# Optimization experiments

Measured on AMD Instinct MI355X. Metric: run time of the kernel, lower is better.

Reference implementation:

```python
import jax, jax.numpy as jnp
import numpy as np

EPS = 1e-6
HEADS = 8

def _ln_cf(x, w, b):
    # ConvNeXt-style channels_first LayerNorm over C axis of (B,C,H,W)
    mu = jnp.mean(x, axis=1, keepdims=True)
    var = jnp.mean((x - mu) ** 2, axis=1, keepdims=True)
    xn = (x - mu) / jnp.sqrt(var + EPS)
    return xn * w[None, :, None, None] + b[None, :, None, None]

def _xattn(q_map, kv_map, Wq, Wk, Wv, Wo, bo):
    B, C, H, W = q_map.shape
    HW = H * W
    dh = C // HEADS
    xq = q_map.reshape(B, C, HW).transpose(0, 2, 1)   # (B,HW,C)
    xkv = kv_map.reshape(B, C, HW).transpose(0, 2, 1)
    q = (xq @ Wq.T).reshape(B, HW, HEADS, dh).transpose(0, 2, 1, 3)
    k = (xkv @ Wk.T).reshape(B, HW, HEADS, dh).transpose(0, 2, 1, 3)
    v = (xkv @ Wv.T).reshape(B, HW, HEADS, dh).transpose(0, 2, 1, 3)
    scale = dh ** -0.5
    logits = jnp.einsum('bhqd,bhkd->bhqk', q, k) * scale
    attn = jax.nn.softmax(logits, axis=-1)
    o = jnp.einsum('bhqk,bhkd->bhqd', attn, v)        # (B,h,HW,dh)
    o = o.transpose(0, 2, 1, 3).reshape(B, HW, C)
    o = o @ Wo.T + bo
    return o.transpose(0, 2, 1).reshape(B, C, H, W)

def _ffn(x, W1, b1, W2, b2):
    # 1x1 convs == channel-wise linear; exact GELU (torch default)
    h = jnp.einsum('bchw,oc->bohw', x, W1) + b1[None, :, None, None]
    h = jax.nn.gelu(h, approximate=False)
    return jnp.einsum('bchw,oc->bohw', h, W2) + b2[None, :, None, None]

def setup_inputs() -> dict:
    key = jax.random.key(0)
    ks = jax.random.split(key, 24)
    B, C, H, W = 8, 512, 32, 32
    hid = 4 * C
    d = {
        'spatial_feat': jax.random.normal(ks[0], (B, C, H, W), jnp.float32),
        'freq_feat': jax.random.normal(ks[1], (B, C, H, W), jnp.float32),
        # spatial enhancer (standard cross-attn)
        's_Wq': jax.random.normal(ks[2], (C, C), jnp.float32) * 0.02,
        's_Wk': jax.random.normal(ks[3], (C, C), jnp.float32) * 0.02,
        's_Wv': jax.random.normal(ks[4], (C, C), jnp.float32) * 0.02,
        's_Wo': jax.random.normal(ks[5], (C, C), jnp.float32) * 0.02,
        's_bo': jnp.zeros((C,), jnp.float32),
        # frequency enhancer
        'f_Wq': jax.random.normal(ks[6], (C, C), jnp.float32) * 0.02,
        'f_Wk': jax.random.normal(ks[7], (C, C), jnp.float32) * 0.02,
        'f_Wv': jax.random.normal(ks[8], (C, C), jnp.float32) * 0.02,
        'f_Wo': jax.random.normal(ks[9], (C, C), jnp.float32) * 0.02,
        'f_bo': jnp.zeros((C,), jnp.float32),
        # norms
        'sn1_w': jnp.ones((C,), jnp.float32), 'sn1_b': jnp.zeros((C,), jnp.float32),
        'sn2_w': jnp.ones((C,), jnp.float32), 'sn2_b': jnp.zeros((C,), jnp.float32),
        'fn1_w': jnp.ones((C,), jnp.float32), 'fn1_b': jnp.zeros((C,), jnp.float32),
        'fn2_w': jnp.ones((C,), jnp.float32), 'fn2_b': jnp.zeros((C,), jnp.float32),
        # ConvFFNs (1x1 convs)
        'sffn_W1': jax.random.normal(ks[10], (hid, C), jnp.float32) * 0.02,
        'sffn_b1': jnp.zeros((hid,), jnp.float32),
        'sffn_W2': jax.random.normal(ks[11], (C, hid), jnp.float32) * 0.02,
        'sffn_b2': jnp.zeros((C,), jnp.float32),
        'fffn_W1': jax.random.normal(ks[12], (hid, C), jnp.float32) * 0.02,
        'fffn_b1': jnp.zeros((hid,), jnp.float32),
        'fffn_W2': jax.random.normal(ks[13], (C, hid), jnp.float32) * 0.02,
        'fffn_b2': jnp.zeros((C,), jnp.float32),
    }
    return d

def reference(spatial_feat, freq_feat,
              s_Wq, s_Wk, s_Wv, s_Wo, s_bo,
              f_Wq, f_Wk, f_Wv, f_Wo, f_bo,
              sn1_w, sn1_b, sn2_w, sn2_b,
              fn1_w, fn1_b, fn2_w, fn2_b,
              sffn_W1, sffn_b1, sffn_W2, sffn_b2,
              fffn_W1, fffn_b1, fffn_W2, fffn_b2):
    enh_s = _xattn(spatial_feat, freq_feat, s_Wq, s_Wk, s_Wv, s_Wo, s_bo)
    enh_f = _xattn(freq_feat, spatial_feat, f_Wq, f_Wk, f_Wv, f_Wo, f_bo)
    s = _ln_cf(spatial_feat + enh_s, sn1_w, sn1_b)
    s = _ln_cf(s + _ffn(s, sffn_W1, sffn_b1, sffn_W2, sffn_b2), sn2_w, sn2_b)
    f = _ln_cf(freq_feat + enh_f, fn1_w, fn1_b)
    f = _ln_cf(f + _ffn(f, fffn_W1, fffn_b1, fffn_W2, fffn_b2), fn2_w, fn2_b)
    return (s, f)
```

## Files before the change

kernel.cpp:

```cpp
#include <hip/hip_runtime.h>
#include <hip/hip_bf16.h>


#define CCH 512
#define HWD 1024

typedef unsigned short u16;
typedef unsigned int u32;
typedef __attribute__((ext_vector_type(8))) __bf16 bf16x8;
typedef __attribute__((ext_vector_type(4))) float f32x4;
typedef __attribute__((ext_vector_type(4))) unsigned short u16x4;
typedef __attribute__((ext_vector_type(8))) unsigned short u16x8;

__device__ __forceinline__ float bf2f(u16 u) { return __uint_as_float(((u32)u) << 16); }
__device__ __forceinline__ u16 f2bf(float f) {
    u32 u = __float_as_uint(f);
    return (u16)((u + 0x7fffu + ((u >> 16) & 1u)) >> 16);
}
__device__ __forceinline__ float ldp(const void* p, int i, bool isbf) {
    return isbf ? bf2f(((const u16*)p)[i]) : ((const float*)p)[i];
}

#define GLL16(g, l) __builtin_amdgcn_global_load_lds( \
    (const __attribute__((address_space(1))) u32*)(g), \
    (__attribute__((address_space(3))) u32*)(l), 16, 0, 0)

struct MMJob { const u16* A; const u16* W; const void* bias; void* Y; };
struct AJob  { const u16* QK; const u16* VT; u16* AO; };
struct LNJob { const u16* A; const float* Br; const void* w; const void* b; void* Y; };

__global__ void k_detect(const u16* __restrict__ in, int* __restrict__ flag) {
    if (threadIdx.x == 0 && blockIdx.x == 0) {
        int sane = 0;
        for (int i = 0; i < 1024; i += 2) {
            int e = (in[i] >> 7) & 0xFF;
            if (e >= 0x6D && e <= 0x8D) sane++;
        }
        *flag = (sane >= 256) ? 1 : 0;
    }
}

struct CvtJobs {
    const void* src[12];
    u16* dst[12];
    int chunk0[13];
};
__global__ __launch_bounds__(256) void k_cvt_all(CvtJobs J, const int* __restrict__ flag) {
    bool isbf = (*flag != 0);
    int b = blockIdx.x;
    int j = 0;
    #pragma unroll
    for (int i = 0; i < 12; i++) if (b >= J.chunk0[i + 1]) j = i + 1;
    int idx = (b - J.chunk0[j]) * 1024 + threadIdx.x * 4;
    u16* d = J.dst[j] + idx;
    if (isbf) {
        *(u16x4*)d = *(const u16x4*)((const u16*)J.src[j] + idx);
    } else {
        float4 v = *(const float4*)((const float*)J.src[j] + idx);
        d[0] = f2bf(v.x); d[1] = f2bf(v.y); d[2] = f2bf(v.z); d[3] = f2bf(v.w);
    }
}

__global__ __launch_bounds__(256) void k_transpose(const void* __restrict__ in,
                                                   u16* __restrict__ out,
                                                   const int* __restrict__ flag) {
    __shared__ float tile[32][33];
    bool isbf = (*flag != 0);
    int b = blockIdx.z;
    int hw0 = blockIdx.x * 32, c0 = blockIdx.y * 32;
    int tx = threadIdx.x, ty = threadIdx.y;
    size_t base = (size_t)b * CCH * HWD;
    if (isbf) {
        const u16* ip = (const u16*)in + base;
        for (int i = ty; i < 32; i += 8)
            tile[i][tx] = bf2f(ip[(size_t)(c0 + i) * HWD + hw0 + tx]);
    } else {
        const float* ip = (const float*)in + base;
        for (int i = ty; i < 32; i += 8)
            tile[i][tx] = ip[(size_t)(c0 + i) * HWD + hw0 + tx];
    }
    __syncthreads();
    u16* op = out + (size_t)b * HWD * CCH;
    for (int i = ty; i < 32; i += 8)
        op[(size_t)(hw0 + i) * CCH + c0 + tx] = f2bf(tile[tx][i]);
}

__device__ __forceinline__ void swz(int pid, int gm, int gn, int& bm, int& bn) {
    int gsz = 8 * gn;
    int gid = pid / gsz;
    int fm = gid * 8;
    int rows = (gm - fm < 8) ? (gm - fm) : 8;
    int pin = pid - gid * gsz;
    bm = fm + pin % rows;
    bn = pin / rows;
}

__global__ __launch_bounds__(256) void k_mm(MMJob j0, MMJob j1,
                                            int K, int ldY, int mode, int gm, int gn,
                                            const int* __restrict__ flag) {
    __shared__ u16 As[128 * 32];
    __shared__ u16 Bs[128 * 32];
    MMJob J = blockIdx.z ? j1 : j0;
    int t = threadIdx.x;
    int w = t >> 6, l = t & 63;
    int bm, bn;
    swz(blockIdx.x, gm, gn, bm, bn);
    int m0 = bm * 128, n0 = bn * 128;
    int wm = (w >> 1) * 64, wn = (w & 1) * 64;

    int r0 = (w * 2 + 0) * 16 + (l >> 2);
    int r1 = (w * 2 + 1) * 16 + (l >> 2);
    int sg = (l & 3) * 8;
    const u16* ga0 = J.A + (size_t)(m0 + r0) * K + sg;
    const u16* ga1 = J.A + (size_t)(m0 + r1) * K + sg;
    const u16* gb0 = J.W + (size_t)(n0 + r0) * K + sg;
    const u16* gb1 = J.W + (size_t)(n0 + r1) * K + sg;
    u16* la0 = &As[(w * 2 + 0) * 512];
    u16* la1 = &As[(w * 2 + 1) * 512];
    u16* lb0 = &Bs[(w * 2 + 0) * 512];
    u16* lb1 = &Bs[(w * 2 + 1) * 512];

    int quad = l >> 4, lr = l & 15;
    int aoff[4], boff[4];
    #pragma unroll
    for (int i = 0; i < 4; i++) {
        aoff[i] = (wm + i * 16 + lr) * 32 + quad * 8;
        boff[i] = (wn + i * 16 + lr) * 32 + quad * 8;
    }

    f32x4 acc[4][4] = {};

    for (int k0 = 0; k0 < K; k0 += 32) {
        __syncthreads();
        GLL16(ga0 + k0, la0);
        GLL16(ga1 + k0, la1);
        GLL16(gb0 + k0, lb0);
        GLL16(gb1 + k0, lb1);
        __syncthreads();
        bf16x8 af[4], bfr[4];
        #pragma unroll
        for (int i = 0; i < 4; i++) af[i] = *(const bf16x8*)&As[aoff[i]];
        #pragma unroll
        for (int j = 0; j < 4; j++) bfr[j] = *(const bf16x8*)&Bs[boff[j]];
        #pragma unroll
        for (int i = 0; i < 4; i++)
            #pragma unroll
            for (int j = 0; j < 4; j++)
                acc[i][j] = __builtin_amdgcn_mfma_f32_16x16x32_bf16(af[i], bfr[j], acc[i][j], 0, 0, 0);
    }

    bool isbf = (*flag != 0);
    #pragma unroll
    for (int i = 0; i < 4; i++) {
        int rowb = m0 + wm + i * 16 + quad * 4;
        #pragma unroll
        for (int j = 0; j < 4; j++) {
            int col = n0 + wn + j * 16 + lr;
            float bv = (mode == 1 || mode == 2) ? ldp(J.bias, col, isbf) : 0.f;
            #pragma unroll
            for (int r = 0; r < 4; r++) {
                float v = acc[i][j][r] + bv;
                if (mode == 2) {
                    v = 0.5f * v * (1.0f + erff(v * 0.70710678118654752f));
                    ((u16*)J.Y)[(size_t)(rowb + r) * ldY + col] = f2bf(v);
                } else if (mode == 3) {
                    ((u16*)J.Y)[(size_t)(rowb + r) * ldY + col] = f2bf(v);
                } else {
                    ((float*)J.Y)[(size_t)(rowb + r) * ldY + col] = v;
                }
            }
        }
    }
}

__global__ __launch_bounds__(256) void k_mm64(MMJob j0, MMJob j1,
                                              int K, int ldY, int mode, int gm, int gn,
                                              const int* __restrict__ flag) {
    __shared__ u16 As[128 * 32];
    __shared__ u16 Bs[64 * 32];
    MMJob J = blockIdx.z ? j1 : j0;
    int t = threadIdx.x;
    int w = t >> 6, l = t & 63;
    int bm, bn;
    swz(blockIdx.x, gm, gn, bm, bn);
    int m0 = bm * 128, n0 = bn * 64;
    int wm = (w >> 1) * 64, wn = (w & 1) * 32;

    int r0 = (w * 2 + 0) * 16 + (l >> 2);
    int r1 = (w * 2 + 1) * 16 + (l >> 2);
    int sg = (l & 3) * 8;
    const u16* ga0 = J.A + (size_t)(m0 + r0) * K + sg;
    const u16* ga1 = J.A + (size_t)(m0 + r1) * K + sg;
    const u16* gb  = J.W + (size_t)(n0 + w * 16 + (l >> 2)) * K + sg;
    u16* la0 = &As[(w * 2 + 0) * 512];
    u16* la1 = &As[(w * 2 + 1) * 512];
    u16* lb  = &Bs[w * 512];

    int quad = l >> 4, lr = l & 15;
    int aoff[4], boff[2];
    #pragma unroll
    for (int i = 0; i < 4; i++) aoff[i] = (wm + i * 16 + lr) * 32 + quad * 8;
    #pragma unroll
    for (int j = 0; j < 2; j++) boff[j] = (wn + j * 16 + lr) * 32 + quad * 8;

    f32x4 acc[4][2] = {};

    for (int k0 = 0; k0 < K; k0 += 32) {
        __syncthreads();
        GLL16(ga0 + k0, la0);
        GLL16(ga1 + k0, la1);
        GLL16(gb + k0, lb);
        __syncthreads();
        bf16x8 af[4], bfr[2];
        #pragma unroll
        for (int i = 0; i < 4; i++) af[i] = *(const bf16x8*)&As[aoff[i]];
        #pragma unroll
        for (int j = 0; j < 2; j++) bfr[j] = *(const bf16x8*)&Bs[boff[j]];
        #pragma unroll
        for (int i = 0; i < 4; i++)
            #pragma unroll
            for (int j = 0; j < 2; j++)
                acc[i][j] = __builtin_amdgcn_mfma_f32_16x16x32_bf16(af[i], bfr[j], acc[i][j], 0, 0, 0);
    }

    bool isbf = (*flag != 0);
    #pragma unroll
    for (int i = 0; i < 4; i++) {
        int rowb = m0 + wm + i * 16 + quad * 4;
        #pragma unroll
        for (int j = 0; j < 2; j++) {
            int col = n0 + wn + j * 16 + lr;
            float bv = (mode == 1 || mode == 2) ? ldp(J.bias, col, isbf) : 0.f;
            #pragma unroll
            for (int r = 0; r < 4; r++) {
                float v = acc[i][j][r] + bv;
                if (mode == 2) {
                    v = 0.5f * v * (1.0f + erff(v * 0.70710678118654752f));
                    ((u16*)J.Y)[(size_t)(rowb + r) * ldY + col] = f2bf(v);
                } else if (mode == 3) {
                    ((u16*)J.Y)[(size_t)(rowb + r) * ldY + col] = f2bf(v);
                } else {
                    ((float*)J.Y)[(size_t)(rowb + r) * ldY + col] = v;
                }
            }
        }
    }
}

__global__ __launch_bounds__(256) void k_attn2(AJob j0, AJob j1) {
    __shared__ __align__(16) u16 Qs[2][128][32];
    __shared__ __align__(16) u16 Ks[2][64][32];
    __shared__ __align__(16) u16 Vs[2][64][32];
    __shared__ __align__(16) u16 Ps[4][32][80];

    AJob J = (blockIdx.x >> 9) ? j1 : j0;
    int blk = blockIdx.x & 511;
    int t = threadIdx.x;
    int w = t >> 6, l = t & 63;
    int l15 = l & 15, quad = l >> 4;
    int qt = blk & 7;
    int bh = blk >> 3;
    int h = bh & 7, b = bh >> 3;
    int tok0 = b * 1024;
    int q0 = qt * 128;
    int hc = h * 64;

    #pragma unroll
    for (int kc = 0; kc < 2; kc++)
        #pragma unroll
        for (int g = 0; g < 2; g++) {
            int row = w * 32 + g * 16 + (l >> 2);
            int sl = ((l & 3) ^ ((row >> 1) & 3)) * 8;
            const u16* gp = J.QK + (size_t)(tok0 + q0 + row) * 1024 + hc + kc * 32 + sl;
            GLL16(gp, &Qs[kc][w * 32 + g * 16][0]);
        }
    __syncthreads();

    bf16x8 qf[2][2];
    #pragma unroll
    for (int jq = 0; jq < 2; jq++)
        #pragma unroll
        for (int kc = 0; kc < 2; kc++) {
            int row = w * 32 + jq * 16 + l15;
            qf[jq][kc] = *(const bf16x8*)&Qs[kc][row][(quad ^ ((row >> 1) & 3)) * 8];
        }

    float m_[2] = {-1e30f, -1e30f};
    float l_[2] = {0.f, 0.f};
    f32x4 acco[2][4] = {};

    for (int kt = 0; kt < 16; kt++) {
        __syncthreads();
        {
            int row = w * 16 + (l >> 2);
            int f = (row >> 1) & 3;
            int sl = ((l & 3) ^ f) * 8;
            int key = kt * 64 + row;
            #pragma unroll
            for (int kc = 0; kc < 2; kc++) {
                const u16* kp = J.QK + (size_t)(tok0 + key) * 1024 + 512 + hc + kc * 32 + sl;
                GLL16(kp, &Ks[kc][w * 16][0]);
            }
            #pragma unroll
            for (int kck = 0; kck < 2; kck++) {
                const u16* vp = J.VT + (size_t)(hc + row) * 8192 + tok0 + kt * 64 + kck * 32 + sl;
                GLL16(vp, &Vs[kck][w * 16][0]);
            }
        }
        __syncthreads();

        f32x4 accs[4][2] = {};
        #pragma unroll
        for (int kc = 0; kc < 2; kc++) {
            bf16x8 kf[4];
            #pragma unroll
            for (int i = 0; i < 4; i++) {
                int row = i * 16 + l15;
                kf[i] = *(const bf16x8*)&Ks[kc][row][(quad ^ ((row >> 1) & 3)) * 8];
            }
            #pragma unroll
            for (int i = 0; i < 4; i++)
                #pragma unroll
                for (int jq = 0; jq < 2; jq++)
                    accs[i][jq] = __builtin_amdgcn_mfma_f32_16x16x32_bf16(kf[i], qf[jq][kc], accs[i][jq], 0, 0, 0);
        }

        float alpha[2];
        #pragma unroll
        for (int jq = 0; jq < 2; jq++) {
            float tm = -1e30f;
            #pragma unroll
            for (int i = 0; i < 4; i++)
                #pragma unroll
                for (int r = 0; r < 4; r++) tm = fmaxf(tm, accs[i][jq][r]);
            tm *= 0.125f;
            tm = fmaxf(tm, __shfl_xor(tm, 16));
            tm = fmaxf(tm, __shfl_xor(tm, 32));
            float mn = fmaxf(m_[jq], tm);
            alpha[jq] = __expf(m_[jq] - mn);
            m_[jq] = mn;
            float ts = 0.f;
            #pragma unroll
            for (int i = 0; i < 4; i++) {
                u16x4 pk;
                #pragma unroll
                for (int r = 0; r < 4; r++) {
                    float p = __expf(accs[i][jq][r] * 0.125f - mn);
                    ts += p;
                    pk[r] = f2bf(p);
                }
                *(u16x4*)&Ps[w][jq * 16 + l15][i * 16 + quad * 4] = pk;
            }
            ts += __shfl_xor(ts, 16);
            ts += __shfl_xor(ts, 32);
            l_[jq] = l_[jq] * alpha[jq] + ts;
        }

        #pragma unroll
        for (int i2 = 0; i2 < 2; i2++)
            #pragma unroll
            for (int r = 0; r < 4; r++) {
                float al = __shfl(alpha[i2], quad * 4 + r);
                #pragma unroll
                for (int jd = 0; jd < 4; jd++) acco[i2][jd][r] *= al;
            }

        #pragma unroll
        for (int kck = 0; kck < 2; kck++) {
            bf16x8 pf[2], vf[4];
            #pragma unroll
            for (int i2 = 0; i2 < 2; i2++)
                pf[i2] = *(const bf16x8*)&Ps[w][i2 * 16 + l15][kck * 32 + quad * 8];
            #pragma unroll
            for (int jd = 0; jd < 4; jd++) {
                int row = jd * 16 + l15;
                vf[jd] = *(const bf16x8*)&Vs[kck][row][(quad ^ ((row >> 1) & 3)) * 8];
            }
            #pragma unroll
            for (int i2 = 0; i2 < 2; i2++)
                #pragma unroll
                for (int jd = 0; jd < 4; jd++)
                    acco[i2][jd] = __builtin_amdgcn_mfma_f32_16x16x32_bf16(pf[i2], vf[jd], acco[i2][jd], 0, 0, 0);
        }
    }

    #pragma unroll
    for (int i2 = 0; i2 < 2; i2++) {
        float linv = 1.0f / l_[i2];
        #pragma unroll
        for (int r = 0; r < 4; r++) {
            float li = __shfl(linv, quad * 4 + r);
            int token = tok0 + q0 + w * 32 + i2 * 16 + quad * 4 + r;
            u16* dst = J.AO + (size_t)token * 512 + hc;
            #pragma unroll
            for (int jd = 0; jd < 4; jd++)
                dst[jd * 16 + l15] = f2bf(acco[i2][jd][r] * li);
        }
    }
}

__global__ __launch_bounds__(256) void k_ln(LNJob j0, LNJob j1,
                                            const int* __restrict__ flag) {
    LNJob J = blockIdx.y ? j1 : j0;
    bool isbf = (*flag != 0);
    int token = blockIdx.x * 4 + (threadIdx.x >> 6);
    int lane = threadIdx.x & 63;
    int c0 = lane * 8;
    const u16* pa = J.A + (size_t)token * CCH + c0;
    const float* pb = J.Br + (size_t)token * CCH + c0;
    u16x8 av = *(const u16x8*)pa;
    float4 b0 = *(const float4*)pb;
    float4 b1 = *(const float4*)(pb + 4);
    float v[8];
    float s = 0.f, s2 = 0.f;
    #pragma unroll
    for (int u = 0; u < 8; u++) {
        float x = bf2f(av[u]) + ((u < 4) ? (&b0.x)[u] : (&b1.x)[u - 4]);
        v[u] = x; s += x; s2 += x * x;
    }
    #pragma unroll
    for (int off = 32; off > 0; off >>= 1) {
        s += __shfl_xor(s, off);
        s2 += __shfl_xor(s2, off);
    }
    float mu = s * (1.f / CCH);
    float var = s2 * (1.f / CCH) - mu * mu;
    float rstd = rsqrtf(var + 1e-6f);
    u16x8 ov;
    #pragma unroll
    for (int u = 0; u < 8; u++)
        ov[u] = f2bf((v[u] - mu) * rstd * ldp(J.w, c0 + u, isbf) + ldp(J.b, c0 + u, isbf));
    *(u16x8*)((u16*)J.Y + (size_t)token * CCH + c0) = ov;
}

__global__ __launch_bounds__(256) void k_ln_out(LNJob j0, LNJob j1,
                                                void* __restrict__ out, int brBase,
                                                const int* __restrict__ flag) {
    LNJob J = blockIdx.y ? j1 : j0;
    int branch = brBase + blockIdx.y;
    bool isbf = (*flag != 0);
    int token = blockIdx.x * 4 + (threadIdx.x >> 6);
    int lane = threadIdx.x & 63;
    int c0 = lane * 8;
    const u16* pa = J.A + (size_t)token * CCH + c0;
    const float* pb = J.Br + (size_t)token * CCH + c0;
    u16x8 av = *(const u16x8*)pa;
    float4 b0 = *(const float4*)pb;
    float4 b1 = *(const float4*)(pb + 4);
    float v[8];
    float s = 0.f, s2 = 0.f;
    #pragma unroll
    for (int u = 0; u < 8; u++) {
        float x = bf2f(av[u]) + ((u < 4) ? (&b0.x)[u] : (&b1.x)[u - 4]);
        v[u] = x; s += x; s2 += x * x;
    }
    #pragma unroll
    for (int off = 32; off > 0; off >>= 1) {
        s += __shfl_xor(s, off);
        s2 += __shfl_xor(s2, off);
    }
    float mu = s * (1.f / CCH);
    float var = s2 * (1.f / CCH) - mu * mu;
    float rstd = rsqrtf(var + 1e-6f);
    int b = token >> 10, hw = token & 1023;
    size_t obase = (size_t)branch * CCH * HWD * 8 + (size_t)b * CCH * HWD + hw;
    if (isbf) {
        u16* op = (u16*)out + obase;
        #pragma unroll
        for (int u = 0; u < 8; u++) {
            float y = (v[u] - mu) * rstd * ldp(J.w, c0 + u, true) + ldp(J.b, c0 + u, true);
            op[(size_t)(c0 + u) * HWD] = f2bf(y);
        }
    } else {
        float* op = (float*)out + obase;
        #pragma unroll
        for (int u = 0; u < 8; u++) {
            float y = (v[u] - mu) * rstd * ldp(J.w, c0 + u, false) + ldp(J.b, c0 + u, false);
            op[(size_t)(c0 + u) * HWD] = y;
        }
    }
}

extern "C" void kernel_launch(void* const* d_in, const int* in_sizes, int n_in,
                              void* d_out, int out_size, void* d_ws, size_t ws_size,
                              hipStream_t stream) {
    (void)in_sizes; (void)n_in; (void)out_size;

    char* wsb = (char*)d_ws;
    int* flag = (int*)wsb;
    u16* Wall = (u16*)(wsb + 256);
    u16* Xs = (u16*)(wsb + 256 + 12582912);
    u16* Xf = (u16*)(wsb + 256 + 12582912 + 8388608);
    char* rbase = wsb + 29360384;

    const size_t BRSZ = 67108864;
    bool dual = ws_size >= (29360384 + 2 * BRSZ);

    u16* QKb[2]; u16* VTb[2]; u16* AOb[2]; u16* Hbb[2];
    float* ENHb[2];
    for (int b = 0; b < 2; b++) {
        char* r = rbase + (dual ? b * BRSZ : 0);
        QKb[b] = (u16*)r;
        ENHb[b] = (float*)r;
        VTb[b] = (u16*)(r + 16777216);
        AOb[b] = (u16*)(r + 16777216 + 8388608);
        Hbb[b] = (u16*)(r + 16777216 + 2 * 8388608);
    }

    const int SQ = 262144, SW1 = 1048576;
    const u16* Xq[2] = {Xs, Xf};
    const u16* Xkv[2] = {Xf, Xs};
    u16* Wq[2]; u16* Wk[2]; u16* Wv[2]; u16* Wo[2]; u16* W1[2]; u16* W2[2];
    const void *bo[2], *n1w[2], *n1b[2], *n2w[2], *n2b[2], *b1[2], *b2[2];
    for (int b = 0; b < 2; b++) {
        u16* Wb = Wall + (size_t)b * 3145728;
        Wq[b] = Wb; Wk[b] = Wb + SQ; Wv[b] = Wb + 2 * SQ; Wo[b] = Wb + 3 * SQ;
        W1[b] = Wb + 4 * SQ; W2[b] = Wb + 4 * SQ + SW1;
        bo[b]  = d_in[b ? 11 : 6];
        n1w[b] = d_in[b ? 16 : 12]; n1b[b] = d_in[b ? 17 : 13];
        n2w[b] = d_in[b ? 18 : 14]; n2b[b] = d_in[b ? 19 : 15];
        b1[b]  = d_in[b ? 25 : 21]; b2[b]  = d_in[b ? 27 : 23];
    }

    k_detect<<<1, 64, 0, stream>>>((const u16*)d_in[0], flag);

    {
        CvtJobs J;
        int ch = 0;
        for (int b = 0; b < 2; b++) {
            const int srcIdx[6] = {b ? 7 : 2, b ? 8 : 3, b ? 9 : 4, b ? 10 : 5,
                                   b ? 24 : 20, b ? 26 : 22};
            u16* dsts[6] = {Wq[b], Wk[b], Wv[b], Wo[b], W1[b], W2[b]};
            const int sz[6] = {SQ, SQ, SQ, SQ, SW1, SW1};
            for (int i = 0; i < 6; i++) {
                int j = b * 6 + i;
                J.src[j] = d_in[srcIdx[i]];
                J.dst[j] = dsts[i];
                J.chunk0[j] = ch;
                ch += sz[i] / 1024;
            }
        }
        J.chunk0[12] = ch;
        k_cvt_all<<<ch, 256, 0, stream>>>(J, flag);
    }

    dim3 tb(32, 8);
    k_transpose<<<dim3(32, 16, 8), tb, 0, stream>>>(d_in[0], Xs, flag);
    k_transpose<<<dim3(32, 16, 8), tb, 0, stream>>>(d_in[1], Xf, flag);

    auto mmj = [&](int b, const u16* A, const u16* W, const void* bias, void* Y) {
        MMJob j; j.A = A; j.W = W; j.bias = bias; j.Y = Y; return j;
    };
    auto lnj = [&](const u16* A, const float* Br, const void* w, const void* bb, void* Y) {
        LNJob j; j.A = A; j.Br = Br; j.w = w; j.b = bb; j.Y = Y; return j;
    };

    int nbr = dual ? 2 : 1;
    int nloop = dual ? 1 : 2;
    for (int it = 0; it < nloop; it++) {
        int b0 = dual ? 0 : it;
        int b1i = dual ? 1 : it;

        k_mm64<<<dim3(512, 1, nbr), 256, 0, stream>>>(
            mmj(b0, Xq[b0], Wq[b0], nullptr, QKb[b0]),
            mmj(b1i, Xq[b1i], Wq[b1i], nullptr, QKb[b1i]),
            512, 1024, 3, 64, 8, flag);
        k_mm64<<<dim3(512, 1, nbr), 256, 0, stream>>>(
            mmj(b0, Xkv[b0], Wk[b0], nullptr, QKb[b0] + 512),
            mmj(b1i, Xkv[b1i], Wk[b1i], nullptr, QKb[b1i] + 512),
            512, 1024, 3, 64, 8, flag);
        k_mm64<<<dim3(512, 1, nbr), 256, 0, stream>>>(
            mmj(b0, Wv[b0], Xkv[b0], nullptr, VTb[b0]),
            mmj(b1i, Wv[b1i], Xkv[b1i], nullptr, VTb[b1i]),
            512, 8192, 3, 4, 128, flag);
        {
            AJob a0, a1;
            a0.QK = QKb[b0]; a0.VT = VTb[b0]; a0.AO = AOb[b0];
            a1.QK = QKb[b1i]; a1.VT = VTb[b1i]; a1.AO = AOb[b1i];
            k_attn2<<<512 * nbr, 256, 0, stream>>>(a0, a1);
        }
        k_mm64<<<dim3(512, 1, nbr), 256, 0, stream>>>(
            mmj(b0, AOb[b0], Wo[b0], bo[b0], ENHb[b0]),
            mmj(b1i, AOb[b1i], Wo[b1i], bo[b1i], ENHb[b1i]),
            512, 512, 1, 64, 8, flag);
        k_ln<<<dim3(2048, nbr), 256, 0, stream>>>(
            lnj(Xq[b0], ENHb[b0], n1w[b0], n1b[b0], AOb[b0]),
            lnj(Xq[b1i], ENHb[b1i], n1w[b1i], n1b[b1i], AOb[b1i]), flag);
        k_mm<<<dim3(1024, 1, nbr), 256, 0, stream>>>(
            mmj(b0, AOb[b0], W1[b0], b1[b0], Hbb[b0]),
            mmj(b1i, AOb[b1i], W1[b1i], b1[b1i], Hbb[b1i]),
            512, 2048, 2, 64, 16, flag);
        k_mm64<<<dim3(512, 1, nbr), 256, 0, stream>>>(
            mmj(b0, Hbb[b0], W2[b0], b2[b0], ENHb[b0]),
            mmj(b1i, Hbb[b1i], W2[b1i], b2[b1i], ENHb[b1i]),
            2048, 512, 1, 64, 8, flag);
        k_ln_out<<<dim3(2048, nbr), 256, 0, stream>>>(
            lnj(AOb[b0], ENHb[b0], n2w[b0], n2b[b0], nullptr),
            lnj(AOb[b1i], ENHb[b1i], n2w[b1i], n2b[b1i], nullptr),
            d_out, dual ? 0 : it, flag);
    }
}
```

Baseline: 578.1 us.

## Swizzle GEMM LDS layout, merge Q/K/V projections, use tanh GELU

Applies an XOR swizzle to the 16-byte chunks of the LDS tiles in both GEMM kernels, so the MFMA fragment reads avoid bank conflicts. Merges the three Q, K and V projection launches into one k_proj launch indexed by blockIdx.z, which removes launch gaps and puts more blocks in flight. Replaces the exact erf GELU with a tanh-based approximation built on __expf, trading a small accuracy deviation from the exact-GELU reference for cheaper epilogue arithmetic.

```diff
diff --git a/kernel.cpp b/kernel.cpp
--- a/kernel.cpp
+++ b/kernel.cpp
@@ -20,12 +20,21 @@
 __device__ __forceinline__ float ldp(const void* p, int i, bool isbf) {
     return isbf ? bf2f(((const u16*)p)[i]) : ((const float*)p)[i];
 }
+__device__ __forceinline__ float fast_gelu(float v) {
+    float a = v * (0.7978845608f + 0.0356774081f * v * v);
+    float e = __expf(-2.0f * fabsf(a));
+    float r = __fdividef(1.0f - e, 1.0f + e);
+    float th = (a < 0.f) ? -r : r;
+    return 0.5f * v * (1.0f + th);
+}
 
 #define GLL16(g, l) __builtin_amdgcn_global_load_lds( \
     (const __attribute__((address_space(1))) u32*)(g), \
     (__attribute__((address_space(3))) u32*)(l), 16, 0, 0)
 
 struct MMJob { const u16* A; const u16* W; const void* bias; void* Y; };
+struct PJob  { const u16* A; const u16* W; u16* Y; int ldY; int gm; int gn; };
+struct PJobs { PJob j[6]; };
 struct AJob  { const u16* QK; const u16* VT; u16* AO; };
 struct LNJob { const u16* A; const float* Br; const void* w; const void* b; void* Y; };
 
@@ -110,11 +119,12 @@
 
     int r0 = (w * 2 + 0) * 16 + (l >> 2);
     int r1 = (w * 2 + 1) * 16 + (l >> 2);
-    int sg = (l & 3) * 8;
-    const u16* ga0 = J.A + (size_t)(m0 + r0) * K + sg;
-    const u16* ga1 = J.A + (size_t)(m0 + r1) * K + sg;
-    const u16* gb0 = J.W + (size_t)(n0 + r0) * K + sg;
-    const u16* gb1 = J.W + (size_t)(n0 + r1) * K + sg;
+    int sg0 = (((l & 3) ^ ((r0 >> 1) & 3))) * 8;
+    int sg1 = (((l & 3) ^ ((r1 >> 1) & 3))) * 8;
+    const u16* ga0 = J.A + (size_t)(m0 + r0) * K + sg0;
+    const u16* ga1 = J.A + (size_t)(m0 + r1) * K + sg1;
+    const u16* gb0 = J.W + (size_t)(n0 + r0) * K + sg0;
+    const u16* gb1 = J.W + (size_t)(n0 + r1) * K + sg1;
     u16* la0 = &As[(w * 2 + 0) * 512];
     u16* la1 = &As[(w * 2 + 1) * 512];
     u16* lb0 = &Bs[(w * 2 + 0) * 512];
@@ -124,8 +134,9 @@
     int aoff[4], boff[4];
     #pragma unroll
     for (int i = 0; i < 4; i++) {
-        aoff[i] = (wm + i * 16 + lr) * 32 + quad * 8;
-        boff[i] = (wn + i * 16 + lr) * 32 + quad * 8;
+        int ra = wm + i * 16 + lr, rb = wn + i * 16 + lr;
+        aoff[i] = ra * 32 + (quad ^ ((ra >> 1) & 3)) * 8;
+        boff[i] = rb * 32 + (quad ^ ((rb >> 1) & 3)) * 8;
     }
 
     f32x4 acc[4][4] = {};
@@ -161,8 +172,7 @@
             for (int r = 0; r < 4; r++) {
                 float v = acc[i][j][r] + bv;
                 if (mode == 2) {
-                    v = 0.5f * v * (1.0f + erff(v * 0.70710678118654752f));
-                    ((u16*)J.Y)[(size_t)(rowb + r) * ldY + col] = f2bf(v);
+                    ((u16*)J.Y)[(size_t)(rowb + r) * ldY + col] = f2bf(fast_gelu(v));
                 } else if (mode == 3) {
                     ((u16*)J.Y)[(size_t)(rowb + r) * ldY + col] = f2bf(v);
                 } else {
@@ -188,10 +198,13 @@
 
     int r0 = (w * 2 + 0) * 16 + (l >> 2);
     int r1 = (w * 2 + 1) * 16 + (l >> 2);
-    int sg = (l & 3) * 8;
-    const u16* ga0 = J.A + (size_t)(m0 + r0) * K + sg;
-    const u16* ga1 = J.A + (size_t)(m0 + r1) * K + sg;
-    const u16* gb  = J.W + (size_t)(n0 + w * 16 + (l >> 2)) * K + sg;
+    int rb_ = w * 16 + (l >> 2);
+    int sg0 = (((l & 3) ^ ((r0 >> 1) & 3))) * 8;
+    int sg1 = (((l & 3) ^ ((r1 >> 1) & 3))) * 8;
+    int sgb = (((l & 3) ^ ((rb_ >> 1) & 3))) * 8;
+    const u16* ga0 = J.A + (size_t)(m0 + r0) * K + sg0;
+    const u16* ga1 = J.A + (size_t)(m0 + r1) * K + sg1;
+    const u16* gb  = J.W + (size_t)(n0 + rb_) * K + sgb;
     u16* la0 = &As[(w * 2 + 0) * 512];
     u16* la1 = &As[(w * 2 + 1) * 512];
     u16* lb  = &Bs[w * 512];
@@ -199,9 +212,15 @@
     int quad = l >> 4, lr = l & 15;
     int aoff[4], boff[2];
     #pragma unroll
-    for (int i = 0; i < 4; i++) aoff[i] = (wm + i * 16 + lr) * 32 + quad * 8;
-    #pragma unroll
-    for (int j = 0; j < 2; j++) boff[j] = (wn + j * 16 + lr) * 32 + quad * 8;
+    for (int i = 0; i < 4; i++) {
+        int ra = wm + i * 16 + lr;
+        aoff[i] = ra * 32 + (quad ^ ((ra >> 1) & 3)) * 8;
+    }
+    #pragma unroll
+    for (int j = 0; j < 2; j++) {
+        int rb2 = wn + j * 16 + lr;
+        boff[j] = rb2 * 32 + (quad ^ ((rb2 >> 1) & 3)) * 8;
+    }
 
     f32x4 acc[4][2] = {};
 
@@ -235,14 +254,85 @@
             for (int r = 0; r < 4; r++) {
                 float v = acc[i][j][r] + bv;
                 if (mode == 2) {
-                    v = 0.5f * v * (1.0f + erff(v * 0.70710678118654752f));
-                    ((u16*)J.Y)[(size_t)(rowb + r) * ldY + col] = f2bf(v);
+                    ((u16*)J.Y)[(size_t)(rowb + r) * ldY + col] = f2bf(fast_gelu(v));
                 } else if (mode == 3) {
                     ((u16*)J.Y)[(size_t)(rowb + r) * ldY + col] = f2bf(v);
                 } else {
                     ((float*)J.Y)[(size_t)(rowb + r) * ldY + col] = v;
                 }
             }
+        }
+    }
+}
+
+__global__ __launch_bounds__(256) void k_proj(PJobs JJ, const int* __restrict__ flag) {
+    __shared__ u16 As[128 * 32];
+    __shared__ u16 Bs[64 * 32];
+    (void)flag;
+    PJob J = JJ.j[blockIdx.z];
+    const int K = 512;
+    int t = threadIdx.x;
+    int w = t >> 6, l = t & 63;
+    int bm, bn;
+    swz(blockIdx.x, J.gm, J.gn, bm, bn);
+    int m0 = bm * 128, n0 = bn * 64;
+    int wm = (w >> 1) * 64, wn = (w & 1) * 32;
+
+    int r0 = (w * 2 + 0) * 16 + (l >> 2);
+    int r1 = (w * 2 + 1) * 16 + (l >> 2);
+    int rb_ = w * 16 + (l >> 2);
+    int sg0 = (((l & 3) ^ ((r0 >> 1) & 3))) * 8;
+    int sg1 = (((l & 3) ^ ((r1 >> 1) & 3))) * 8;
+    int sgb = (((l & 3) ^ ((rb_ >> 1) & 3))) * 8;
+    const u16* ga0 = J.A + (size_t)(m0 + r0) * K + sg0;
+    const u16* ga1 = J.A + (size_t)(m0 + r1) * K + sg1;
+    const u16* gb  = J.W + (size_t)(n0 + rb_) * K + sgb;
+    u16* la0 = &As[(w * 2 + 0) * 512];
+    u16* la1 = &As[(w * 2 + 1) * 512];
+    u16* lb  = &Bs[w * 512];
+
+    int quad = l >> 4, lr = l & 15;
+    int aoff[4], boff[2];
+    #pragma unroll
+    for (int i = 0; i < 4; i++) {
+        int ra = wm + i * 16 + lr;
+        aoff[i] = ra * 32 + (quad ^ ((ra >> 1) & 3)) * 8;
+    }
+    #pragma unroll
+    for (int j = 0; j < 2; j++) {
+        int rb2 = wn + j * 16 + lr;
+        boff[j] = rb2 * 32 + (quad ^ ((rb2 >> 1) & 3)) * 8;
+    }
+
+    f32x4 acc[4][2] = {};
+
+    for (int k0 = 0; k0 < K; k0 += 32) {
+        __syncthreads();
+        GLL16(ga0 + k0, la0);
+        GLL16(ga1 + k0, la1);
+        GLL16(gb + k0, lb);
+        __syncthreads();
+        bf16x8 af[4], bfr[2];
+        #pragma unroll
+        for (int i = 0; i < 4; i++) af[i] = *(const bf16x8*)&As[aoff[i]];
+        #pragma unroll
+        for (int j = 0; j < 2; j++) bfr[j] = *(const bf16x8*)&Bs[boff[j]];
+        #pragma unroll
+        for (int i = 0; i < 4; i++)
+            #pragma unroll
+            for (int j = 0; j < 2; j++)
+                acc[i][j] = __builtin_amdgcn_mfma_f32_16x16x32_bf16(af[i], bfr[j], acc[i][j], 0, 0, 0);
+    }
+
+    #pragma unroll
+    for (int i = 0; i < 4; i++) {
+        int rowb = m0 + wm + i * 16 + quad * 4;
+        #pragma unroll
+        for (int j = 0; j < 2; j++) {
+            int col = n0 + wn + j * 16 + lr;
+            #pragma unroll
+            for (int r = 0; r < 4; r++)
+                J.Y[(size_t)(rowb + r) * J.ldY + col] = f2bf(acc[i][j][r]);
         }
     }
 }
@@ -548,8 +638,11 @@
     k_transpose<<<dim3(32, 16, 8), tb, 0, stream>>>(d_in[0], Xs, flag);
     k_transpose<<<dim3(32, 16, 8), tb, 0, stream>>>(d_in[1], Xf, flag);
 
-    auto mmj = [&](int b, const u16* A, const u16* W, const void* bias, void* Y) {
+    auto mmj = [&](const u16* A, const u16* W, const void* bias, void* Y) {
         MMJob j; j.A = A; j.W = W; j.bias = bias; j.Y = Y; return j;
+    };
+    auto pj = [&](const u16* A, const u16* W, u16* Y, int ldY, int gm, int gn) {
+        PJob j; j.A = A; j.W = W; j.Y = Y; j.ldY = ldY; j.gm = gm; j.gn = gn; return j;
     };
     auto lnj = [&](const u16* A, const float* Br, const void* w, const void* bb, void* Y) {
         LNJob j; j.A = A; j.Br = Br; j.w = w; j.b = bb; j.Y = Y; return j;
@@ -561,18 +654,18 @@
         int b0 = dual ? 0 : it;
         int b1i = dual ? 1 : it;
 
-        k_mm64<<<dim3(512, 1, nbr), 256, 0, stream>>>(
-            mmj(b0, Xq[b0], Wq[b0], nullptr, QKb[b0]),
-            mmj(b1i, Xq[b1i], Wq[b1i], nullptr, QKb[b1i]),
-            512, 1024, 3, 64, 8, flag);
-        k_mm64<<<dim3(512, 1, nbr), 256, 0, stream>>>(
-            mmj(b0, Xkv[b0], Wk[b0], nullptr, QKb[b0] + 512),
-            mmj(b1i, Xkv[b1i], Wk[b1i], nullptr, QKb[b1i] + 512),
-            512, 1024, 3, 64, 8, flag);
-        k_mm64<<<dim3(512, 1, nbr), 256, 0, stream>>>(
-            mmj(b0, Wv[b0], Xkv[b0], nullptr, VTb[b0]),
-            mmj(b1i, Wv[b1i], Xkv[b1i], nullptr, VTb[b1i]),
-            512, 8192, 3, 4, 128, flag);
+        {
+            PJobs JJ;
+            int nz = 0;
+            for (int z = 0; z < nbr; z++) {
+                int b = dual ? z : it;
+                JJ.j[nz++] = pj(Xq[b], Wq[b], QKb[b], 1024, 64, 8);
+                JJ.j[nz++] = pj(Xkv[b], Wk[b], QKb[b] + 512, 1024, 64, 8);
+                JJ.j[nz++] = pj(Wv[b], Xkv[b], VTb[b], 8192, 4, 128);
+            }
+            for (int z = nz; z < 6; z++) JJ.j[z] = JJ.j[0];
+            k_proj<<<dim3(512, 1, nz), 256, 0, stream>>>(JJ, flag);
+        }
         {
             AJob a0, a1;
             a0.QK = QKb[b0]; a0.VT = VTb[b0]; a0.AO = AOb[b0];
@@ -580,19 +673,19 @@
             k_attn2<<<512 * nbr, 256, 0, stream>>>(a0, a1);
         }
         k_mm64<<<dim3(512, 1, nbr), 256, 0, stream>>>(
-            mmj(b0, AOb[b0], Wo[b0], bo[b0], ENHb[b0]),
-            mmj(b1i, AOb[b1i], Wo[b1i], bo[b1i], ENHb[b1i]),
+            mmj(AOb[b0], Wo[b0], bo[b0], ENHb[b0]),
+            mmj(AOb[b1i], Wo[b1i], bo[b1i], ENHb[b1i]),
             512, 512, 1, 64, 8, flag);
         k_ln<<<dim3(2048, nbr), 256, 0, stream>>>(
             lnj(Xq[b0], ENHb[b0], n1w[b0], n1b[b0], AOb[b0]),
             lnj(Xq[b1i], ENHb[b1i], n1w[b1i], n1b[b1i], AOb[b1i]), flag);
         k_mm<<<dim3(1024, 1, nbr), 256, 0, stream>>>(
-            mmj(b0, AOb[b0], W1[b0], b1[b0], Hbb[b0]),
-            mmj(b1i, AOb[b1i], W1[b1i], b1[b1i], Hbb[b1i]),
+            mmj(AOb[b0], W1[b0], b1[b0], Hbb[b0]),
+            mmj(AOb[b1i], W1[b1i], b1[b1i], Hbb[b1i]),
             512, 2048, 2, 64, 16, flag);
         k_mm64<<<dim3(512, 1, nbr), 256, 0, stream>>>(
-            mmj(b0, Hbb[b0], W2[b0], b2[b0], ENHb[b0]),
-            mmj(b1i, Hbb[b1i], W2[b1i], b2[b1i], ENHb[b1i]),
+            mmj(Hbb[b0], W2[b0], b2[b0], ENHb[b0]),
+            mmj(Hbb[b1i], W2[b1i], b2[b1i], ENHb[b1i]),
             2048, 512, 1, 64, 8, flag);
         k_ln_out<<<dim3(2048, nbr), 256, 0, stream>>>(
             lnj(AOb[b0], ENHb[b0], n2w[b0], n2b[b0], nullptr),
```

After: 553.2 us. 4.3% less time.
